# Kernel optimization log

Hardware: AMD Instinct MI355X
Metric: run time of the kernel (lower is better)

Reference implementation:

```python
import jax, jax.numpy as jnp
import numpy as np

B, F, N, H = 2, 32, 1024, 64

def setup_inputs() -> dict:
    key = jax.random.key(0)
    ks = jax.random.split(key, 6)
    adj_in = jax.random.normal(ks[0], (B, N, N), dtype=jnp.float32)
    emb_in = jax.random.normal(ks[1], (B, F, N), dtype=jnp.float32)
    # torch Linear default init ~ U(-1/sqrt(fan_in), 1/sqrt(fan_in)); any scale works for a reference
    W1 = jax.random.normal(ks[2], (H, 2 * F), dtype=jnp.float32) * (1.0 / np.sqrt(2 * F))
    b1 = jax.random.normal(ks[3], (H,), dtype=jnp.float32) * (1.0 / np.sqrt(2 * F))
    W2 = jax.random.normal(ks[4], (1, H), dtype=jnp.float32) * (1.0 / np.sqrt(H))
    b2 = jax.random.normal(ks[5], (1,), dtype=jnp.float32) * (1.0 / np.sqrt(H))
    return {"adj_in": adj_in, "emb_in": emb_in, "layer": 0,
            "W1": W1, "b1": b1, "W2": W2, "b2": b2}

def reference(adj_in, emb_in, layer, W1, b1, W2, b2):
    # emb_in: [B, F, N] -> e: [B, N, F]
    e = jnp.swapaxes(emb_in, 1, 2)
    fmaps = e.shape[-1]
    # cartesian row (i*N + j) = concat(e[i], e[j]); split W1 over the two halves
    # so we never materialize the [B, N*N, 2F] concat tensor.
    W1a, W1b = W1[:, :fmaps], W1[:, fmaps:]
    hi = jnp.einsum('bnf,hf->bnh', e, W1a)  # contribution of node i (row)
    hj = jnp.einsum('bnf,hf->bnh', e, W1b)  # contribution of node j (col)
    h = jax.nn.relu(hi[:, :, None, :] + hj[:, None, :, :] + b1)  # [B, N, N, H]
    logits = jnp.einsum('bijh,h->bij', h, W2[0]) + b2[0]          # [B, N, N]
    return jax.nn.sigmoid(logits)
```

## Files before the change

kernel.cpp:

```cpp
#include <hip/hip_runtime.h>
#include <hip/hip_bf16.h>
#include <math.h>

#define BB 2
#define FF 32
#define NN 1024
#define HH 64
#define TI 8

__global__ __launch_bounds__(256) void prep_kernel(
    const float* __restrict__ emb,
    const float* __restrict__ W1,
    const float* __restrict__ b1,
    float* __restrict__ hi,
    float* __restrict__ hjb)
{
    int t = blockIdx.x * 256 + threadIdx.x;
    int h = t & (HH - 1);
    int n = (t >> 6) & (NN - 1);
    int b = t >> 16;

    const float* e = emb + (size_t)b * FF * NN + n;
    const float* w = W1 + (size_t)h * (2 * FF);

    float si = 0.f, sj = 0.f;
#pragma unroll
    for (int f = 0; f < FF; ++f) {
        float ev = e[(size_t)f * NN];
        si = fmaf(ev, w[f], si);
        sj = fmaf(ev, w[FF + f], sj);
    }
    hi[t]  = si;
    hjb[t] = sj + b1[h];
}

__global__ __launch_bounds__(256) void edge_kernel(
    const float* __restrict__ hi,
    const float* __restrict__ hjb,
    const float* __restrict__ W2,
    const float* __restrict__ b2,
    float* __restrict__ out)
{
    const int j  = blockIdx.x * 256 + threadIdx.x;
    const int i0 = blockIdx.y * TI;
    const int b  = blockIdx.z;

    float4 hjr[16];
    const float4* hjp = (const float4*)(hjb + ((size_t)b * NN + j) * HH);
#pragma unroll
    for (int k = 0; k < 16; ++k) hjr[k] = hjp[k];

    const float b2v = b2[0];
    const float* hib = hi + ((size_t)b * NN + i0) * HH;
    float* op = out + ((size_t)b * NN + i0) * NN + j;

#pragma unroll
    for (int ii = 0; ii < TI; ++ii) {
        const float* hirow = hib + ii * HH;
        float a0 = 0.f, a1 = 0.f, a2 = 0.f, a3 = 0.f;
#pragma unroll
        for (int k = 0; k < 16; ++k) {
            const float4 hj4 = hjr[k];
            float h0 = fmaxf(hj4.x + hirow[4 * k + 0], 0.f);
            float h1 = fmaxf(hj4.y + hirow[4 * k + 1], 0.f);
            float h2 = fmaxf(hj4.z + hirow[4 * k + 2], 0.f);
            float h3 = fmaxf(hj4.w + hirow[4 * k + 3], 0.f);
            a0 = fmaf(h0, W2[4 * k + 0], a0);
            a1 = fmaf(h1, W2[4 * k + 1], a1);
            a2 = fmaf(h2, W2[4 * k + 2], a2);
            a3 = fmaf(h3, W2[4 * k + 3], a3);
        }
        float s = (a0 + a1) + (a2 + a3) + b2v;
        op[(size_t)ii * NN] = 1.0f / (1.0f + __expf(-s));
    }
}

extern "C" void kernel_launch(void* const* d_in, const int* in_sizes, int n_in,
                              void* d_out, int out_size, void* d_ws, size_t ws_size,
                              hipStream_t stream) {
    const float* emb = (const float*)d_in[1];
    const float* W1  = (const float*)d_in[3];
    const float* b1  = (const float*)d_in[4];
    const float* W2  = (const float*)d_in[5];
    const float* b2  = (const float*)d_in[6];
    float* out = (float*)d_out;

    float* hi  = (float*)d_ws;
    float* hjb = hi + (size_t)BB * NN * HH;

    prep_kernel<<<(BB * NN * HH) / 256, 256, 0, stream>>>(emb, W1, b1, hi, hjb);

    dim3 grid(NN / 256, NN / TI, BB);
    edge_kernel<<<grid, 256, 0, stream>>>(hi, hjb, W2, b2, out);
}
```

Measured before the change: 97.65 us.

## Use packed fp16 add/relu and fdot2 in edge kernel with folded W2 scaling

Stores hi and hj+b1 as fp16, prescaled by |W2[h]|, so the edge kernel can do packed half2 add and relu and accumulate with fdot2 against a ±log2(e) sign vector. This halves the ALU op count per hidden unit and halves the register and load footprint. The sigmoid uses native exp2 and rcp with the log2(e) factor folded in. The cost is reduced precision: fp16 sums and relu lose accuracy compared with the fp32 reference, and the |W2| folding assumes relu(x)*|w| equals relu(x*|w|), which holds.

```diff
diff --git a/kernel.cpp b/kernel.cpp
--- a/kernel.cpp
+++ b/kernel.cpp
@@ -1,5 +1,4 @@
 #include <hip/hip_runtime.h>
-#include <hip/hip_bf16.h>
 #include <math.h>
 
 #define BB 2
@@ -8,12 +7,16 @@
 #define HH 64
 #define TI 8
 
+typedef _Float16 h2 __attribute__((ext_vector_type(2)));
+
 __global__ __launch_bounds__(256) void prep_kernel(
     const float* __restrict__ emb,
     const float* __restrict__ W1,
     const float* __restrict__ b1,
-    float* __restrict__ hi,
-    float* __restrict__ hjb)
+    const float* __restrict__ W2,
+    _Float16* __restrict__ hi2,
+    _Float16* __restrict__ hjb2,
+    _Float16* __restrict__ wpk)
 {
     int t = blockIdx.x * 256 + threadIdx.x;
     int h = t & (HH - 1);
@@ -30,14 +33,16 @@
         si = fmaf(ev, w[f], si);
         sj = fmaf(ev, w[FF + f], sj);
     }
-    hi[t]  = si;
-    hjb[t] = sj + b1[h];
+    float aw = fabsf(W2[h]);
+    hi2[t]  = (_Float16)(si * aw);
+    hjb2[t] = (_Float16)((sj + b1[h]) * aw);
+    if (t < HH) wpk[t] = (_Float16)copysignf(1.44269504f, W2[t]);
 }
 
 __global__ __launch_bounds__(256) void edge_kernel(
-    const float* __restrict__ hi,
-    const float* __restrict__ hjb,
-    const float* __restrict__ W2,
+    const _Float16* __restrict__ hi2,
+    const _Float16* __restrict__ hjb2,
+    const _Float16* __restrict__ wpk,
     const float* __restrict__ b2,
     float* __restrict__ out)
 {
@@ -45,33 +50,46 @@
     const int i0 = blockIdx.y * TI;
     const int b  = blockIdx.z;
 
-    float4 hjr[16];
-    const float4* hjp = (const float4*)(hjb + ((size_t)b * NN + j) * HH);
+    float4 hjv[8];
+    const float4* hp = (const float4*)(hjb2 + ((size_t)b * NN + j) * HH);
 #pragma unroll
-    for (int k = 0; k < 16; ++k) hjr[k] = hjp[k];
+    for (int k = 0; k < 8; ++k) hjv[k] = hp[k];
+    const h2* hj = (const h2*)hjv;
 
-    const float b2v = b2[0];
-    const float* hib = hi + ((size_t)b * NN + i0) * HH;
+    float4 wv[8];
+    const float4* wp = (const float4*)wpk;
+#pragma unroll
+    for (int k = 0; k < 8; ++k) wv[k] = wp[k];
+    const h2* wh = (const h2*)wv;
+
+    const float accInit = b2[0] * 1.44269504f;
+    const _Float16* hib = hi2 + ((size_t)b * NN + i0) * HH;
     float* op = out + ((size_t)b * NN + i0) * NN + j;
+
+    const h2 hz = { _Float16(0), _Float16(0) };
 
 #pragma unroll
     for (int ii = 0; ii < TI; ++ii) {
-        const float* hirow = hib + ii * HH;
-        float a0 = 0.f, a1 = 0.f, a2 = 0.f, a3 = 0.f;
+        float4 hiv[8];
+        const float4* hr = (const float4*)(hib + (size_t)ii * HH);
 #pragma unroll
-        for (int k = 0; k < 16; ++k) {
-            const float4 hj4 = hjr[k];
-            float h0 = fmaxf(hj4.x + hirow[4 * k + 0], 0.f);
-            float h1 = fmaxf(hj4.y + hirow[4 * k + 1], 0.f);
-            float h2 = fmaxf(hj4.z + hirow[4 * k + 2], 0.f);
-            float h3 = fmaxf(hj4.w + hirow[4 * k + 3], 0.f);
-            a0 = fmaf(h0, W2[4 * k + 0], a0);
-            a1 = fmaf(h1, W2[4 * k + 1], a1);
-            a2 = fmaf(h2, W2[4 * k + 2], a2);
-            a3 = fmaf(h3, W2[4 * k + 3], a3);
+        for (int k = 0; k < 8; ++k) hiv[k] = hr[k];
+        const h2* hih = (const h2*)hiv;
+
+        float a0 = accInit, a1 = 0.f, a2 = 0.f, a3 = 0.f;
+#pragma unroll
+        for (int k = 0; k < 8; ++k) {
+            h2 t0 = __builtin_elementwise_max(hih[4 * k + 0] + hj[4 * k + 0], hz);
+            h2 t1 = __builtin_elementwise_max(hih[4 * k + 1] + hj[4 * k + 1], hz);
+            h2 t2 = __builtin_elementwise_max(hih[4 * k + 2] + hj[4 * k + 2], hz);
+            h2 t3 = __builtin_elementwise_max(hih[4 * k + 3] + hj[4 * k + 3], hz);
+            a0 = __builtin_amdgcn_fdot2(t0, wh[4 * k + 0], a0, false);
+            a1 = __builtin_amdgcn_fdot2(t1, wh[4 * k + 1], a1, false);
+            a2 = __builtin_amdgcn_fdot2(t2, wh[4 * k + 2], a2, false);
+            a3 = __builtin_amdgcn_fdot2(t3, wh[4 * k + 3], a3, false);
         }
-        float s = (a0 + a1) + (a2 + a3) + b2v;
-        op[(size_t)ii * NN] = 1.0f / (1.0f + __expf(-s));
+        float s = (a0 + a1) + (a2 + a3);
+        op[(size_t)ii * NN] = __builtin_amdgcn_rcpf(1.f + __builtin_amdgcn_exp2f(-s));
     }
 }
 
@@ -85,11 +103,12 @@
     const float* b2  = (const float*)d_in[6];
     float* out = (float*)d_out;
 
-    float* hi  = (float*)d_ws;
-    float* hjb = hi + (size_t)BB * NN * HH;
+    _Float16* hi2  = (_Float16*)d_ws;
+    _Float16* hjb2 = hi2 + (size_t)BB * NN * HH;
+    _Float16* wpk  = hjb2 + (size_t)BB * NN * HH;
 
-    prep_kernel<<<(BB * NN * HH) / 256, 256, 0, stream>>>(emb, W1, b1, hi, hjb);
+    prep_kernel<<<(BB * NN * HH) / 256, 256, 0, stream>>>(emb, W1, b1, W2, hi2, hjb2, wpk);
 
     dim3 grid(NN / 256, NN / TI, BB);
-    edge_kernel<<<grid, 256, 0, stream>>>(hi, hjb, W2, b2, out);
+    edge_kernel<<<grid, 256, 0, stream>>>(hi2, hjb2, wpk, b2, out);
 }
```

Result: faster. 85.26 us (-12.7%).
